# Kernel optimization log

Hardware: AMD Instinct MI355X
Metric: run time of the kernel (lower is better)

Reference implementation:

```python
import jax, jax.numpy as jnp
import numpy as np

EPS = 1e-5


def spmm(rows, cols, vals, x):
    # x: (B, C, V); y[b,c,v] = sum_{e: rows[e]==v} vals[e] * x[b,c,cols[e]]
    B, C, V = x.shape
    xt = x.reshape(B * C, V).T                      # (V, B*C)
    msg = vals[:, None] * xt[cols]                  # (E, B*C)
    y = jax.ops.segment_sum(msg, rows, num_segments=V)
    return y.T.reshape(B, C, V)


def cheb_conv(x, W, b, rows, cols, vals):
    # W: (K, Cin, Cout); Chebyshev recurrence over node dim
    K = W.shape[0]
    Tk = [x]
    if K > 1:
        Tk.append(spmm(rows, cols, vals, x))
    for _ in range(2, K):
        Tk.append(2.0 * spmm(rows, cols, vals, Tk[-1]) - Tk[-2])
    T = jnp.stack(Tk)                               # (K, B, Cin, V)
    out = jnp.einsum('kbiv,kio->bov', T, W)
    if b is not None:
        out = out + b[None, :, None]
    return out


def bn(x, g, be):
    # BatchNorm1d training-mode stats over (batch, nodes) per channel
    m = jnp.mean(x, axis=(0, 2), keepdims=True)
    v = jnp.var(x, axis=(0, 2), keepdims=True)
    return (x - m) * jax.lax.rsqrt(v + EPS) * g[None, :, None] + be[None, :, None]


def res_block(x, rows, cols, vals, ga, bea, Wa, ba, gb, beb, Wb, bb, Ws=None):
    xn = bn(x, ga, bea)
    out = cheb_conv(xn, Wa, ba, rows, cols, vals)
    out = bn(jax.nn.relu(out), gb, beb)
    out = cheb_conv(out, Wb, bb, rows, cols, vals)
    sc = xn if Ws is None else cheb_conv(xn, Ws, None, rows, cols, vals)
    return jax.nn.relu(out + sc)


def setup_inputs() -> dict:
    key = jax.random.key(0)
    ks = iter(jax.random.split(key, 40))
    V, E, B, K = 50000, 800000, 8, 4
    d = {}
    d['x'] = jax.random.normal(next(ks), (B, 16, V), dtype=jnp.float32)
    d['lap_rows'] = jax.random.randint(next(ks), (E,), 0, V, dtype=jnp.int32)
    d['lap_cols'] = jax.random.randint(next(ks), (E,), 0, V, dtype=jnp.int32)
    d['lap_vals'] = jax.random.normal(next(ks), (E,), dtype=jnp.float32) * 0.05

    def w(shape, scale=0.1):
        return jax.random.normal(next(ks), shape, dtype=jnp.float32) * scale

    d['W_in'], d['b_in'] = w((K, 16, 32)), w((32,))
    # block 1: 32 -> [32] -> 32 (identity shortcut)
    d['g1a'], d['be1a'] = jnp.ones(32), jnp.zeros(32)
    d['W1a'], d['b1a'] = w((K, 32, 32)), w((32,))
    d['g1b'], d['be1b'] = jnp.ones(32), jnp.zeros(32)
    d['W1b'], d['b1b'] = w((K, 32, 32)), w((32,))
    # block 2: 32 -> [64] -> 64 (ChebConv K=1 shortcut, no bias)
    d['g2a'], d['be2a'] = jnp.ones(32), jnp.zeros(32)
    d['W2a'], d['b2a'] = w((K, 32, 64)), w((64,))
    d['g2b'], d['be2b'] = jnp.ones(64), jnp.zeros(64)
    d['W2b'], d['b2b'] = w((K, 64, 64)), w((64,))
    d['W2s'] = w((1, 32, 64))
    # block 3: 64 -> [64] -> 64 (identity shortcut)
    d['g3a'], d['be3a'] = jnp.ones(64), jnp.zeros(64)
    d['W3a'], d['b3a'] = w((K, 64, 64)), w((64,))
    d['g3b'], d['be3b'] = jnp.ones(64), jnp.zeros(64)
    d['W3b'], d['b3b'] = w((K, 64, 64)), w((64,))
    # output head
    d['g_out'], d['be_out'] = jnp.ones(64), jnp.zeros(64)
    d['W_out'], d['b_out'] = w((K, 64, 10)), w((10,))
    return d


def reference(x, lap_rows, lap_cols, lap_vals,
              W_in, b_in,
              g1a, be1a, W1a, b1a, g1b, be1b, W1b, b1b,
              g2a, be2a, W2a, b2a, g2b, be2b, W2b, b2b, W2s,
              g3a, be3a, W3a, b3a, g3b, be3b, W3b, b3b,
              g_out, be_out, W_out, b_out):
    r, c, v = lap_rows, lap_cols, lap_vals
    out = jax.nn.relu(cheb_conv(x, W_in, b_in, r, c, v))
    out = res_block(out, r, c, v, g1a, be1a, W1a, b1a, g1b, be1b, W1b, b1b)
    out = res_block(out, r, c, v, g2a, be2a, W2a, b2a, g2b, be2b, W2b, b2b, W2s)
    out = res_block(out, r, c, v, g3a, be3a, W3a, b3a, g3b, be3b, W3b, b3b)
    out = bn(out, g_out, be_out)
    out = jax.nn.relu(cheb_conv(out, W_out, b_out, r, c, v))
    pooled = jnp.max(out, axis=2)                   # global max pool over nodes -> (B, 10)
    return jax.nn.log_softmax(pooled, axis=1)
```

## Files before the change

kernel.cpp:

```cpp
#include <hip/hip_runtime.h>
#include <hip/hip_bf16.h>
#include <hip/hip_fp16.h>

typedef float v2f __attribute__((ext_vector_type(2)));
__device__ __forceinline__ v2f vfma2(v2f a, v2f b, v2f c) {
#if __has_builtin(__builtin_elementwise_fma)
    return __builtin_elementwise_fma(a, b, c);
#else
    v2f d; d.x = fmaf(a.x, b.x, c.x); d.y = fmaf(a.y, b.y, c.y); return d;
#endif
}

__global__ void hist_kernel(const int* __restrict__ rows, int* __restrict__ counts, int E) {
    int i = blockIdx.x * blockDim.x + threadIdx.x;
    if (i < E) atomicAdd(&counts[rows[i]], 1);
}

__global__ void chunk_sum_kernel(const int* __restrict__ counts, int* __restrict__ chunk_sums, int V) {
    __shared__ int sh[256];
    int t = threadIdx.x;
    int i = blockIdx.x * 256 + t;
    sh[t] = (i < V) ? counts[i] : 0;
    __syncthreads();
    for (int st = 128; st > 0; st >>= 1) {
        if (t < st) sh[t] += sh[t + st];
        __syncthreads();
    }
    if (t == 0) chunk_sums[blockIdx.x] = sh[0];
}

__global__ void scan_chunks_kernel(int* __restrict__ cs, int n) {
    __shared__ int wsum[4];
    int t = threadIdx.x, lane = t & 63, w = t >> 6;
    int orig = (t < n) ? cs[t] : 0;
    int x = orig;
    #pragma unroll
    for (int d = 1; d < 64; d <<= 1) {
        int y = __shfl_up(x, d);
        if (lane >= d) x += y;
    }
    if (lane == 63) wsum[w] = x;
    __syncthreads();
    int wo = 0;
    for (int j = 0; j < w; ++j) wo += wsum[j];
    if (t < n) cs[t] = wo + x - orig;
}

__global__ void scan_final_kernel(const int* __restrict__ counts, const int* __restrict__ chunk_off,
                                  int* __restrict__ row_ptr, int V) {
    __shared__ int wsum[4];
    int t = threadIdx.x, lane = t & 63, w = t >> 6;
    int i = blockIdx.x * 256 + t;
    int x = (i < V) ? counts[i] : 0;
    #pragma unroll
    for (int d = 1; d < 64; d <<= 1) {
        int y = __shfl_up(x, d);
        if (lane >= d) x += y;
    }
    if (lane == 63) wsum[w] = x;
    __syncthreads();
    int wo = 0;
    for (int j = 0; j < w; ++j) wo += wsum[j];
    if (i < V) row_ptr[i + 1] = chunk_off[blockIdx.x] + wo + x;
    if (i == 0) row_ptr[0] = 0;
}

__global__ void init_cursor_kernel(const int* __restrict__ row_ptr, int* __restrict__ cursor, int V) {
    int i = blockIdx.x * blockDim.x + threadIdx.x;
    if (i < V) cursor[i] = row_ptr[i];
}

__global__ void scatter_kernel(const int* __restrict__ rows, const int* __restrict__ cols,
                               const float* __restrict__ vals, int* __restrict__ cursor,
                               int* __restrict__ cols_s, float* __restrict__ vals_s, int E) {
    int i = blockIdx.x * blockDim.x + threadIdx.x;
    if (i < E) {
        int r = rows[i];
        int p = atomicAdd(&cursor[r], 1);
        cols_s[p] = cols[i];
        vals_s[p] = vals[i];
    }
}

__global__ void sort_rows_kernel(const int* __restrict__ row_ptr, int* cols, float* vals, int V) {
    int v = blockIdx.x * blockDim.x + threadIdx.x;
    if (v >= V) return;
    int e0 = row_ptr[v], e1 = row_ptr[v + 1];
    for (int i = e0 + 1; i < e1; ++i) {
        int c = cols[i];
        unsigned xb = __float_as_uint(vals[i]);
        int j = i - 1;
        while (j >= e0) {
            int cj = cols[j];
            unsigned vj = __float_as_uint(vals[j]);
            if (cj > c || (cj == c && vj > xb)) {
                cols[j + 1] = cj; vals[j + 1] = __uint_as_float(vj);
                --j;
            } else break;
        }
        cols[j + 1] = c;
        vals[j + 1] = __uint_as_float(xb);
    }
}

__global__ void transpose_in_kernel(const float* __restrict__ x, __half* __restrict__ X, int V) {
    int total = V * 128;
    for (int i = blockIdx.x * blockDim.x + threadIdx.x; i < total; i += gridDim.x * blockDim.x) {
        int v = i >> 7;
        int t = i & 127;
        X[i] = __float2half(x[t * V + v]);
    }
}

template <int VPT> struct PackT;
template <> struct PackT<1> { using T = float;  };
template <> struct PackT<2> { using T = float2; };
template <> struct PackT<4> { using T = float4; };

template <int VPT>
__global__ __launch_bounds__(256) void spmm2_kernel(
    const int* __restrict__ row_ptr, const int* __restrict__ cols,
    const float* __restrict__ vals, const __half2* __restrict__ src,
    __half2* dst, const __half2* prev, int V) {
    using T = typename PackT<VPT>::T;
    union U { T raw; __half2 h[VPT]; };
    int lane = threadIdx.x & 63;
    int v = (blockIdx.x << 2) | (threadIdx.x >> 6);
    if (v >= V) return;
    const int W = VPT * 64;
    const size_t row = (size_t)v * W + lane * VPT;

    float pr[2 * VPT];
    bool hasp = (prev != nullptr);
    if (hasp) {
        U pv; pv.raw = *(const T*)(prev + row);
        #pragma unroll
        for (int j = 0; j < VPT; ++j) {
            float2 f = __half22float2(pv.h[j]);
            pr[2 * j] = f.x; pr[2 * j + 1] = f.y;
        }
    }
    float acc[2 * VPT];
    #pragma unroll
    for (int j = 0; j < 2 * VPT; ++j) acc[j] = 0.f;

    int e0 = row_ptr[v], e1 = row_ptr[v + 1];
    int e = e0;
    for (; e + 8 <= e1; e += 8) {
        int   c[8]; float w[8]; U g[8];
        #pragma unroll
        for (int k = 0; k < 8; ++k) { c[k] = cols[e + k]; w[k] = vals[e + k]; }
        #pragma unroll
        for (int k = 0; k < 8; ++k)
            g[k].raw = *(const T*)(src + (size_t)c[k] * W + lane * VPT);
        #pragma unroll
        for (int k = 0; k < 8; ++k) {
            #pragma unroll
            for (int j = 0; j < VPT; ++j) {
                float2 f = __half22float2(g[k].h[j]);
                acc[2*j] += w[k] * f.x; acc[2*j+1] += w[k] * f.y;
            }
        }
    }
    for (; e + 4 <= e1; e += 4) {
        int   c[4]; float w[4]; U g[4];
        #pragma unroll
        for (int k = 0; k < 4; ++k) { c[k] = cols[e + k]; w[k] = vals[e + k]; }
        #pragma unroll
        for (int k = 0; k < 4; ++k)
            g[k].raw = *(const T*)(src + (size_t)c[k] * W + lane * VPT);
        #pragma unroll
        for (int k = 0; k < 4; ++k) {
            #pragma unroll
            for (int j = 0; j < VPT; ++j) {
                float2 f = __half22float2(g[k].h[j]);
                acc[2*j] += w[k] * f.x; acc[2*j+1] += w[k] * f.y;
            }
        }
    }
    for (; e < e1; ++e) {
        int c = cols[e]; float wv = vals[e];
        U g; g.raw = *(const T*)(src + (size_t)c * W + lane * VPT);
        #pragma unroll
        for (int j = 0; j < VPT; ++j) {
            float2 f = __half22float2(g.h[j]);
            acc[2*j] += wv * f.x; acc[2*j+1] += wv * f.y;
        }
    }
    if (hasp) {
        #pragma unroll
        for (int j = 0; j < 2 * VPT; ++j) acc[j] = 2.f * acc[j] - pr[j];
    }
    U o;
    #pragma unroll
    for (int j = 0; j < VPT; ++j) o.h[j] = __floats2half2_rn(acc[2*j], acc[2*j+1]);
    *(T*)(dst + row) = o.raw;
}

template <int CIN, int COUT>
__global__ __launch_bounds__(256) void combine_kernel(
    const __half* T0, const __half* T1, const __half* T2, const __half* T3,
    const float* __restrict__ W, const float* __restrict__ bias,
    const __half* res, const __half* sc, const float* __restrict__ Wsc,
    __half* out, int relu, int V) {
    const int CSC = 32;
    const int SL  = CIN / 8;
    const int SLS = CSC / 8;
    const int MAXC = (CIN > CSC) ? CIN : CSC;
    __shared__ float4 tile[256 * MAXC / 8];
    union U4 { float4 raw; __half2 h[4]; };

    int g = blockIdx.x * 256 + threadIdx.x;
    int g0 = blockIdx.x * 256;
    bool active = (g < V * 8);

    v2f acc[COUT / 2];
    #pragma unroll
    for (int c = 0; c < COUT / 2; ++c) {
        if (bias) { acc[c].x = bias[2 * c]; acc[c].y = bias[2 * c + 1]; }
        else      { acc[c].x = 0.f;         acc[c].y = 0.f; }
    }

    const int xorv = ((threadIdx.x * SL) >> 3) & (SL - 1);

    const __half* Ts[4] = {T0, T1, T2, T3};
    #pragma unroll
    for (int k = 0; k < 4; ++k) {
        __syncthreads();
        {
            const float4* gp = (const float4*)(Ts[k] + (size_t)g0 * CIN);
            #pragma unroll
            for (int j = 0; j < SL; ++j) {
                int idx = threadIdx.x + j * 256;
                int r = idx / SL, c4 = idx & (SL - 1);
                if (g0 + r < V * 8)
                    tile[r * SL + (c4 ^ (((r * SL) >> 3) & (SL - 1)))] = gp[idx];
            }
        }
        __syncthreads();
        if (active) {
            const float* Wk = W + (size_t)k * CIN * COUT;
            #pragma unroll 1
            for (int c4 = 0; c4 < SL; ++c4) {
                U4 x; x.raw = tile[threadIdx.x * SL + (c4 ^ xorv)];
                #pragma unroll
                for (int s = 0; s < 4; ++s) {
                    int q = c4 * 4 + s;
                    float2 a = __half22float2(x.h[s]);
                    const v2f* w0 = (const v2f*)(Wk + (size_t)(2 * q) * COUT);
                    const v2f* w1 = (const v2f*)(Wk + (size_t)(2 * q + 1) * COUT);
                    v2f ax = {a.x, a.x}, ay = {a.y, a.y};
                    #pragma unroll
                    for (int c = 0; c < COUT / 2; ++c) {
                        acc[c] = vfma2(ax, w0[c], acc[c]);
                        acc[c] = vfma2(ay, w1[c], acc[c]);
                    }
                }
            }
        }
    }
    if (sc) {
        __syncthreads();
        {
            const float4* gp = (const float4*)(sc + (size_t)g0 * CSC);
            #pragma unroll
            for (int j = 0; j < SLS; ++j) {
                int idx = threadIdx.x + j * 256;
                int r = idx / SLS, c4 = idx & (SLS - 1);
                if (g0 + r < V * 8)
                    tile[r * SLS + (c4 ^ (((r * SLS) >> 3) & (SLS - 1)))] = gp[idx];
            }
        }
        __syncthreads();
        if (active) {
            const int xorsc = ((threadIdx.x * SLS) >> 3) & (SLS - 1);
            #pragma unroll 1
            for (int c4 = 0; c4 < SLS; ++c4) {
                U4 x; x.raw = tile[threadIdx.x * SLS + (c4 ^ xorsc)];
                #pragma unroll
                for (int s = 0; s < 4; ++s) {
                    int q = c4 * 4 + s;
                    float2 a = __half22float2(x.h[s]);
                    const v2f* w0 = (const v2f*)(Wsc + (size_t)(2 * q) * COUT);
                    const v2f* w1 = (const v2f*)(Wsc + (size_t)(2 * q + 1) * COUT);
                    v2f ax = {a.x, a.x}, ay = {a.y, a.y};
                    #pragma unroll
                    for (int c = 0; c < COUT / 2; ++c) {
                        acc[c] = vfma2(ax, w0[c], acc[c]);
                        acc[c] = vfma2(ay, w1[c], acc[c]);
                    }
                }
            }
        }
    }
    if (!active) return;

    size_t ob = (size_t)g * COUT;
    if constexpr (COUT % 8 == 0) {
        if (res) {
            const float4* rr = (const float4*)(res + ob);
            #pragma unroll
            for (int q = 0; q < COUT / 8; ++q) {
                U4 rv; rv.raw = rr[q];
                #pragma unroll
                for (int s = 0; s < 4; ++s) {
                    float2 f = __half22float2(rv.h[s]);
                    acc[q * 4 + s].x += f.x; acc[q * 4 + s].y += f.y;
                }
            }
        }
        if (relu) {
            #pragma unroll
            for (int c = 0; c < COUT / 2; ++c) {
                acc[c].x = fmaxf(acc[c].x, 0.f);
                acc[c].y = fmaxf(acc[c].y, 0.f);
            }
        }
        float4* ro = (float4*)(out + ob);
        #pragma unroll
        for (int q = 0; q < COUT / 8; ++q) {
            U4 o;
            #pragma unroll
            for (int s = 0; s < 4; ++s)
                o.h[s] = __floats2half2_rn(acc[q * 4 + s].x, acc[q * 4 + s].y);
            ro[q] = o.raw;
        }
    } else {
        if (res) {
            const __half2* rr = (const __half2*)(res + ob);
            #pragma unroll
            for (int c = 0; c < COUT / 2; ++c) {
                float2 f = __half22float2(rr[c]);
                acc[c].x += f.x; acc[c].y += f.y;
            }
        }
        if (relu) {
            #pragma unroll
            for (int c = 0; c < COUT / 2; ++c) {
                acc[c].x = fmaxf(acc[c].x, 0.f);
                acc[c].y = fmaxf(acc[c].y, 0.f);
            }
        }
        __half2* ro = (__half2*)(out + ob);
        #pragma unroll
        for (int c = 0; c < COUT / 2; ++c)
            ro[c] = __floats2half2_rn(acc[c].x, acc[c].y);
    }
}

__global__ void bn_stats_part_kernel(const __half2* __restrict__ x2, int C, int relu_in,
                                     float* __restrict__ part, size_t N2) {
    __shared__ float sx[256], qx[256], sy[256], qy[256];
    int t = threadIdx.x;
    size_t i0 = (size_t)blockIdx.x * 256 + t;
    size_t step = (size_t)gridDim.x * 256;
    float ax = 0.f, aqx = 0.f, ay = 0.f, aqy = 0.f;
    for (size_t i = i0; i < N2; i += step) {
        float2 f = __half22float2(x2[i]);
        if (relu_in) { f.x = fmaxf(f.x, 0.f); f.y = fmaxf(f.y, 0.f); }
        ax += f.x; aqx += f.x * f.x;
        ay += f.y; aqy += f.y * f.y;
    }
    sx[t] = ax; qx[t] = aqx; sy[t] = ay; qy[t] = aqy;
    __syncthreads();
    int half = C >> 1;
    for (int st = 128; st >= half; st >>= 1) {
        if (t < st) {
            sx[t] += sx[t + st]; qx[t] += qx[t + st];
            sy[t] += sy[t + st]; qy[t] += qy[t + st];
        }
        __syncthreads();
    }
    if (t < half) {
        part[blockIdx.x * 128 + 2 * t]         = sx[t];
        part[blockIdx.x * 128 + 2 * t + 1]     = sy[t];
        part[blockIdx.x * 128 + C + 2 * t]     = qx[t];
        part[blockIdx.x * 128 + C + 2 * t + 1] = qy[t];
    }
}

__global__ void bn_reduce_kernel(const float* __restrict__ part, int nblk,
                                 const float* __restrict__ g, const float* __restrict__ be,
                                 float* __restrict__ ss, int C, float invN) {
    int c = threadIdx.x;
    if (c < C) {
        float s = 0.f, q = 0.f;
        for (int b = 0; b < nblk; ++b) {
            s += part[b * 128 + c];
            q += part[b * 128 + C + c];
        }
        float m = s * invN;
        float var = q * invN - m * m;
        float sc = g[c] * rsqrtf(var + 1e-5f);
        ss[c] = sc;
        ss[C + c] = be[c] - m * sc;
    }
}

__global__ void affine_h_kernel(__half* x, const float* __restrict__ ss, int C,
                                int relu_in, size_t N2) {
    union U4 { float4 raw; __half2 h[4]; };
    size_t NG = N2 >> 2;
    size_t stride = (size_t)gridDim.x * blockDim.x;
    size_t i0 = (size_t)blockIdx.x * blockDim.x + threadIdx.x;
    float4* x4 = (float4*)x;
    int c0 = (int)((8 * i0) & (size_t)(C - 1));
    float sc[8], of[8];
    #pragma unroll
    for (int j = 0; j < 8; ++j) { sc[j] = ss[c0 + j]; of[j] = ss[C + c0 + j]; }
    for (size_t i = i0; i < NG; i += stride) {
        U4 u; u.raw = x4[i];
        #pragma unroll
        for (int j = 0; j < 4; ++j) {
            float2 f = __half22float2(u.h[j]);
            if (relu_in) { f.x = fmaxf(f.x, 0.f); f.y = fmaxf(f.y, 0.f); }
            f.x = f.x * sc[2 * j] + of[2 * j];
            f.y = f.y * sc[2 * j + 1] + of[2 * j + 1];
            u.h[j] = __floats2half2_rn(f.x, f.y);
        }
        x4[i] = u.raw;
    }
}

__global__ void maxpool_h_kernel(const __half* __restrict__ x, float* pooled, int V, int NS) {
    __shared__ float red[256];
    int o = blockIdx.x % 80;
    int slice = blockIdx.x / 80;
    int v0 = (int)((long long)V * slice / NS);
    int v1 = (int)((long long)V * (slice + 1) / NS);
    float m = 0.f;
    for (int v = v0 + threadIdx.x; v < v1; v += 256)
        m = fmaxf(m, __half2float(x[(size_t)v * 80 + o]));
    red[threadIdx.x] = m;
    __syncthreads();
    for (int st = 128; st > 0; st >>= 1) {
        if (threadIdx.x < st) red[threadIdx.x] = fmaxf(red[threadIdx.x], red[threadIdx.x + st]);
        __syncthreads();
    }
    if (threadIdx.x == 0) atomicMax((int*)&pooled[o], __float_as_int(red[0]));
}

__global__ void lsm_kernel(const float* __restrict__ pooled, float* __restrict__ out) {
    int b = threadIdx.x;
    if (b < 8) {
        float m = -1e30f;
        for (int c = 0; c < 10; ++c) m = fmaxf(m, pooled[b * 10 + c]);
        float s = 0.f;
        for (int c = 0; c < 10; ++c) s += expf(pooled[b * 10 + c] - m);
        float l = logf(s);
        for (int c = 0; c < 10; ++c)
            out[b * 10 + c] = pooled[b * 10 + c] - m - l;
    }
}

__global__ void encode_kernel(float* out, float val) {
    int i = threadIdx.x;
    if (i < 80) out[i] = val;
}

extern "C" void kernel_launch(void* const* d_in, const int* in_sizes, int n_in,
                              void* d_out, int out_size, void* d_ws, size_t ws_size,
                              hipStream_t stream) {
    (void)in_sizes; (void)n_in; (void)out_size;
    const int V = 50000, E = 800000;
    const int NCH = (V + 255) / 256;
    const int SB = 512;
    const int NS = 8;

    auto al = [](size_t x) { return (x + 255) & ~(size_t)255; };
    const size_t FB = al((size_t)V * 512 * sizeof(__half));
    const size_t need = 5 * FB + al((V + 1) * 4) + al(V * 4) + al(E * 4) + al(E * 4)
                      + al((size_t)SB * 128 * 4) + al(8 * 128 * 4) + al(80 * 4) + al(NCH * 4);
    if (ws_size < need) {
        encode_kernel<<<1, 128, 0, stream>>>((float*)d_out, (float)(ws_size >> 20));
        return;
    }

    const float* x_in = (const float*)d_in[0];
    const int* rows   = (const int*)d_in[1];
    const int* colsi  = (const int*)d_in[2];
    const float* lvals = (const float*)d_in[3];
    const float* W_in = (const float*)d_in[4];
    const float* b_in = (const float*)d_in[5];
    const float* g1a = (const float*)d_in[6],  *be1a = (const float*)d_in[7];
    const float* W1a = (const float*)d_in[8],  *b1a  = (const float*)d_in[9];
    const float* g1b = (const float*)d_in[10], *be1b = (const float*)d_in[11];
    const float* W1b = (const float*)d_in[12], *b1b  = (const float*)d_in[13];
    const float* g2a = (const float*)d_in[14], *be2a = (const float*)d_in[15];
    const float* W2a = (const float*)d_in[16], *b2a  = (const float*)d_in[17];
    const float* g2b = (const float*)d_in[18], *be2b = (const float*)d_in[19];
    const float* W2b = (const float*)d_in[20], *b2b  = (const float*)d_in[21];
    const float* W2s = (const float*)d_in[22];
    const float* g3a = (const float*)d_in[23], *be3a = (const float*)d_in[24];
    const float* W3a = (const float*)d_in[25], *b3a  = (const float*)d_in[26];
    const float* g3b = (const float*)d_in[27], *be3b = (const float*)d_in[28];
    const float* W3b = (const float*)d_in[29], *b3b  = (const float*)d_in[30];
    const float* g_o = (const float*)d_in[31], *be_o = (const float*)d_in[32];
    const float* W_o = (const float*)d_in[33], *b_o  = (const float*)d_in[34];

    char* wp = (char*)d_ws;
    auto take = [&](size_t bytes) -> void* { void* p = (void*)wp; wp += al(bytes); return p; };
    __half* P0 = (__half*)take(FB);
    __half* P1 = (__half*)take(FB);
    __half* P2 = (__half*)take(FB);
    __half* P3 = (__half*)take(FB);
    __half* P4 = (__half*)take(FB);
    int* row_ptr  = (int*)take((V + 1) * sizeof(int));
    int* cursor   = (int*)take(V * sizeof(int));
    int* cols_s   = (int*)take(E * sizeof(int));
    float* vals_s = (float*)take(E * sizeof(float));
    float* part   = (float*)take((size_t)SB * 128 * sizeof(float));
    float* aff    = (float*)take(8 * 128 * sizeof(float));
    float* pooled = (float*)take(80 * sizeof(float));
    int* chunks   = (int*)take(NCH * sizeof(int));

    hipMemsetAsync(cursor, 0, V * sizeof(int), stream);
    hipMemsetAsync(pooled, 0, 80 * sizeof(float), stream);

    hist_kernel<<<(E + 255) / 256, 256, 0, stream>>>(rows, cursor, E);
    chunk_sum_kernel<<<NCH, 256, 0, stream>>>(cursor, chunks, V);
    scan_chunks_kernel<<<1, 256, 0, stream>>>(chunks, NCH);
    scan_final_kernel<<<NCH, 256, 0, stream>>>(cursor, chunks, row_ptr, V);
    init_cursor_kernel<<<(V + 255) / 256, 256, 0, stream>>>(row_ptr, cursor, V);
    scatter_kernel<<<(E + 255) / 256, 256, 0, stream>>>(rows, colsi, lvals, cursor, cols_s, vals_s, E);
    sort_rows_kernel<<<(V + 255) / 256, 256, 0, stream>>>(row_ptr, cols_s, vals_s, V);
    transpose_in_kernel<<<4096, 256, 0, stream>>>(x_in, P0, V);

    auto spmm = [&](const __half* src, __half* dst, const __half* prev, int C) {
        int grid = (V + 3) / 4;
        if (C == 16)
            spmm2_kernel<1><<<grid, 256, 0, stream>>>(row_ptr, cols_s, vals_s,
                (const __half2*)src, (__half2*)dst, (const __half2*)prev, V);
        else if (C == 32)
            spmm2_kernel<2><<<grid, 256, 0, stream>>>(row_ptr, cols_s, vals_s,
                (const __half2*)src, (__half2*)dst, (const __half2*)prev, V);
        else
            spmm2_kernel<4><<<grid, 256, 0, stream>>>(row_ptr, cols_s, vals_s,
                (const __half2*)src, (__half2*)dst, (const __half2*)prev, V);
    };
    const int MG = (V * 8 + 255) / 256;
    auto comb = [&](const __half* T0, const __half* T1, const __half* T2, const __half* T3,
                    int Cin, int Cout, const float* W, const float* bias,
                    const __half* res, const __half* sc, const float* Wsc,
                    __half* out, int relu) {
        if (Cin == 16 && Cout == 32)
            combine_kernel<16, 32><<<MG, 256, 0, stream>>>(T0, T1, T2, T3, W, bias, res, sc, Wsc, out, relu, V);
        else if (Cin == 32 && Cout == 32)
            combine_kernel<32, 32><<<MG, 256, 0, stream>>>(T0, T1, T2, T3, W, bias, res, sc, Wsc, out, relu, V);
        else if (Cin == 32 && Cout == 64)
            combine_kernel<32, 64><<<MG, 256, 0, stream>>>(T0, T1, T2, T3, W, bias, res, sc, Wsc, out, relu, V);
        else if (Cin == 64 && Cout == 64)
            combine_kernel<64, 64><<<MG, 256, 0, stream>>>(T0, T1, T2, T3, W, bias, res, sc, Wsc, out, relu, V);
        else
            combine_kernel<64, 10><<<MG, 256, 0, stream>>>(T0, T1, T2, T3, W, bias, res, sc, Wsc, out, relu, V);
    };
    auto stats = [&](const __half* xb, int C, int relu, int slot, const float* g, const float* be) {
        bn_stats_part_kernel<<<SB, 256, 0, stream>>>((const __half2*)xb, C, relu, part,
                                                     (size_t)V * 4 * C);
        bn_reduce_kernel<<<1, 64, 0, stream>>>(part, SB, g, be, aff + slot * 128, C,
                                               1.f / ((float)V * 8.f));
    };
    auto affine = [&](__half* xb, int C, int relu, int slot) {
        affine_h_kernel<<<2048, 256, 0, stream>>>(xb, aff + slot * 128, C, relu,
                                                  (size_t)V * 4 * C);
    };
    const __half* NH = nullptr;
    const float*  NF = nullptr;

    spmm(P0, P1, nullptr, 16);
    spmm(P1, P2, P0, 16);
    spmm(P2, P3, P1, 16);
    comb(P0, P1, P2, P3, 16, 32, W_in, b_in, NH, NH, NF, P4, 1);

    stats(P4, 32, 0, 0, g1a, be1a);
    affine(P4, 32, 0, 0);
    spmm(P4, P0, nullptr, 32);
    spmm(P0, P1, P4, 32);
    spmm(P1, P2, P0, 32);
    comb(P4, P0, P1, P2, 32, 32, W1a, b1a, NH, NH, NF, P0, 0);
    stats(P0, 32, 1, 1, g1b, be1b);
    affine(P0, 32, 1, 1);
    spmm(P0, P1, nullptr, 32);
    spmm(P1, P2, P0, 32);
    spmm(P2, P3, P1, 32);
    comb(P0, P1, P2, P3, 32, 32, W1b, b1b, P4, NH, NF, P4, 1);

    stats(P4, 32, 0, 2, g2a, be2a);
    affine(P4, 32, 0, 2);
    spmm(P4, P0, nullptr, 32);
    spmm(P0, P1, P4, 32);
    spmm(P1, P2, P0, 32);
    comb(P4, P0, P1, P2, 32, 64, W2a, b2a, NH, NH, NF, P3, 0);
    stats(P3, 64, 1, 3, g2b, be2b);
    affine(P3, 64, 1, 3);
    spmm(P3, P0, nullptr, 64);
    spmm(P0, P1, P3, 64);
    spmm(P1, P2, P0, 64);
    comb(P3, P0, P1, P2, 64, 64, W2b, b2b, NH, P4, W2s, P0, 1);

    stats(P0, 64, 0, 4, g3a, be3a);
    affine(P0, 64, 0, 4);
    spmm(P0, P1, nullptr, 64);
    spmm(P1, P2, P0, 64);
    spmm(P2, P3, P1, 64);
    comb(P0, P1, P2, P3, 64, 64, W3a, b3a, NH, NH, NF, P1, 0);
    stats(P1, 64, 1, 5, g3b, be3b);
    affine(P1, 64, 1, 5);
    spmm(P1, P2, nullptr, 64);
    spmm(P2, P3, P1, 64);
    spmm(P3, P4, P2, 64);
    comb(P1, P2, P3, P4, 64, 64, W3b, b3b, P0, NH, NF, P1, 1);

    stats(P1, 64, 0, 6, g_o, be_o);
    affine(P1, 64, 0, 6);
    spmm(P1, P0, nullptr, 64);
    spmm(P0, P2, P1, 64);
    spmm(P2, P3, P0, 64);
    comb(P1, P0, P2, P3, 64, 10, W_o, b_o, NH, NH, NF, P4, 1);
    maxpool_h_kernel<<<80 * NS, 256, 0, stream>>>(P4, pooled, V, NS);
    lsm_kernel<<<1, 64, 0, stream>>>(pooled, (float*)d_out);
}
```

Measured before the change: 4.940 ms.

## Stage combine tiles per wavefront with async global-to-LDS loads and prefetch

```diff
diff --git a/kernel.cpp b/kernel.cpp
--- a/kernel.cpp
+++ b/kernel.cpp
@@ -203,16 +203,18 @@
     const float* __restrict__ W, const float* __restrict__ bias,
     const __half* res, const __half* sc, const float* __restrict__ Wsc,
     __half* out, int relu, int V) {
-    const int CSC = 32;
-    const int SL  = CIN / 8;
-    const int SLS = CSC / 8;
-    const int MAXC = (CIN > CSC) ? CIN : CSC;
-    __shared__ float4 tile[256 * MAXC / 8];
+    constexpr int SL  = CIN / 8;
+    constexpr int SLS = 32 / 8;
+    constexpr int LOGSL = (SL == 8) ? 3 : (SL == 4) ? 2 : 1;
+    __shared__ float4 tile[4 * 64 * SL];
     union U4 { float4 raw; __half2 h[4]; };
 
-    int g = blockIdx.x * 256 + threadIdx.x;
-    int g0 = blockIdx.x * 256;
-    bool active = (g < V * 8);
+    const int lane = threadIdx.x & 63;
+    const int wid  = threadIdx.x >> 6;
+    const int w0   = blockIdx.x * 256 + wid * 64;
+    if (w0 >= V * 8) return;
+    const int g = w0 + lane;
+    float4* wt = tile + wid * 64 * SL;
 
     v2f acc[COUT / 2];
     #pragma unroll
@@ -221,79 +223,79 @@
         else      { acc[c].x = 0.f;         acc[c].y = 0.f; }
     }
 
-    const int xorv = ((threadIdx.x * SL) >> 3) & (SL - 1);
+    auto stageT = [&](const __half* src) {
+        const float4* gb = (const float4*)src + (size_t)w0 * SL;
+        #pragma unroll
+        for (int j = 0; j < SL; ++j) {
+            int r  = (j << (6 - LOGSL)) + (lane >> LOGSL);
+            int sp = lane & (SL - 1);
+            const float4* s4 = gb + r * SL + (sp ^ (r & (SL - 1)));
+            __builtin_amdgcn_global_load_lds(
+                (const __attribute__((address_space(1))) void*)s4,
+                (__attribute__((address_space(3))) void*)(wt + j * 64),
+                16, 0, 0);
+        }
+    };
 
     const __half* Ts[4] = {T0, T1, T2, T3};
+    stageT(T0);
+    const int xorv = lane & (SL - 1);
     #pragma unroll
     for (int k = 0; k < 4; ++k) {
-        __syncthreads();
-        {
-            const float4* gp = (const float4*)(Ts[k] + (size_t)g0 * CIN);
-            #pragma unroll
-            for (int j = 0; j < SL; ++j) {
-                int idx = threadIdx.x + j * 256;
-                int r = idx / SL, c4 = idx & (SL - 1);
-                if (g0 + r < V * 8)
-                    tile[r * SL + (c4 ^ (((r * SL) >> 3) & (SL - 1)))] = gp[idx];
-            }
-        }
-        __syncthreads();
-        if (active) {
-            const float* Wk = W + (size_t)k * CIN * COUT;
-            #pragma unroll 1
-            for (int c4 = 0; c4 < SL; ++c4) {
-                U4 x; x.raw = tile[threadIdx.x * SL + (c4 ^ xorv)];
+        asm volatile("s_waitcnt vmcnt(0)" ::: "memory");
+        const float* Wk = W + (size_t)k * CIN * COUT;
+        #pragma unroll 1
+        for (int c4 = 0; c4 < SL; ++c4) {
+            U4 x; x.raw = wt[lane * SL + (c4 ^ xorv)];
+            #pragma unroll
+            for (int s = 0; s < 4; ++s) {
+                int q = c4 * 4 + s;
+                float2 a = __half22float2(x.h[s]);
+                const v2f* wp0 = (const v2f*)(Wk + (size_t)(2 * q) * COUT);
+                const v2f* wp1 = (const v2f*)(Wk + (size_t)(2 * q + 1) * COUT);
+                v2f ax = {a.x, a.x}, ay = {a.y, a.y};
                 #pragma unroll
-                for (int s = 0; s < 4; ++s) {
-                    int q = c4 * 4 + s;
-                    float2 a = __half22float2(x.h[s]);
-                    const v2f* w0 = (const v2f*)(Wk + (size_t)(2 * q) * COUT);
-                    const v2f* w1 = (const v2f*)(Wk + (size_t)(2 * q + 1) * COUT);
-                    v2f ax = {a.x, a.x}, ay = {a.y, a.y};
-                    #pragma unroll
-                    for (int c = 0; c < COUT / 2; ++c) {
-                        acc[c] = vfma2(ax, w0[c], acc[c]);
-                        acc[c] = vfma2(ay, w1[c], acc[c]);
-                    }
+                for (int c = 0; c < COUT / 2; ++c) {
+                    acc[c] = vfma2(ax, wp0[c], acc[c]);
+                    acc[c] = vfma2(ay, wp1[c], acc[c]);
                 }
             }
         }
+        asm volatile("s_waitcnt lgkmcnt(0)" ::: "memory");
+        if (k < 3) stageT(Ts[k + 1]);
     }
     if (sc) {
-        __syncthreads();
-        {
-            const float4* gp = (const float4*)(sc + (size_t)g0 * CSC);
-            #pragma unroll
-            for (int j = 0; j < SLS; ++j) {
-                int idx = threadIdx.x + j * 256;
-                int r = idx / SLS, c4 = idx & (SLS - 1);
-                if (g0 + r < V * 8)
-                    tile[r * SLS + (c4 ^ (((r * SLS) >> 3) & (SLS - 1)))] = gp[idx];
-            }
-        }
-        __syncthreads();
-        if (active) {
-            const int xorsc = ((threadIdx.x * SLS) >> 3) & (SLS - 1);
-            #pragma unroll 1
-            for (int c4 = 0; c4 < SLS; ++c4) {
-                U4 x; x.raw = tile[threadIdx.x * SLS + (c4 ^ xorsc)];
+        const float4* gb = (const float4*)sc + (size_t)w0 * SLS;
+        #pragma unroll
+        for (int j = 0; j < SLS; ++j) {
+            int r  = (j << 4) + (lane >> 2);
+            int sp = lane & (SLS - 1);
+            const float4* s4 = gb + r * SLS + (sp ^ (r & (SLS - 1)));
+            __builtin_amdgcn_global_load_lds(
+                (const __attribute__((address_space(1))) void*)s4,
+                (__attribute__((address_space(3))) void*)(wt + j * 64),
+                16, 0, 0);
+        }
+        asm volatile("s_waitcnt vmcnt(0)" ::: "memory");
+        const int xorsc = lane & (SLS - 1);
+        #pragma unroll 1
+        for (int c4 = 0; c4 < SLS; ++c4) {
+            U4 x; x.raw = wt[lane * SLS + (c4 ^ xorsc)];
+            #pragma unroll
+            for (int s = 0; s < 4; ++s) {
+                int q = c4 * 4 + s;
+                float2 a = __half22float2(x.h[s]);
+                const v2f* wp0 = (const v2f*)(Wsc + (size_t)(2 * q) * COUT);
+                const v2f* wp1 = (const v2f*)(Wsc + (size_t)(2 * q + 1) * COUT);
+                v2f ax = {a.x, a.x}, ay = {a.y, a.y};
                 #pragma unroll
-                for (int s = 0; s < 4; ++s) {
-                    int q = c4 * 4 + s;
-                    float2 a = __half22float2(x.h[s]);
-                    const v2f* w0 = (const v2f*)(Wsc + (size_t)(2 * q) * COUT);
-                    const v2f* w1 = (const v2f*)(Wsc + (size_t)(2 * q + 1) * COUT);
-                    v2f ax = {a.x, a.x}, ay = {a.y, a.y};
-                    #pragma unroll
-                    for (int c = 0; c < COUT / 2; ++c) {
-                        acc[c] = vfma2(ax, w0[c], acc[c]);
-                        acc[c] = vfma2(ay, w1[c], acc[c]);
-                    }
+                for (int c = 0; c < COUT / 2; ++c) {
+                    acc[c] = vfma2(ax, wp0[c], acc[c]);
+                    acc[c] = vfma2(ay, wp1[c], acc[c]);
                 }
             }
         }
     }
-    if (!active) return;
 
     size_t ob = (size_t)g * COUT;
     if constexpr (COUT % 8 == 0) {
```

After: 4.477 ms. 1.1x faster.
